# Kernel tuning notes

Measured on AMD Instinct MI355X. Metric: run time of the kernel, lower is better.

The kernel has to match this reference:

```python
import jax, jax.numpy as jnp
import numpy as np

HIDDEN = 16
PROJ = 2
INPUT = 2


def _gates_split(gates):
    # PyTorch LSTM gate order: input, forget, cell(g), output
    i, f, g, o = jnp.split(gates, 4, axis=-1)
    return jax.nn.sigmoid(i), jax.nn.sigmoid(f), jnp.tanh(g), jax.nn.sigmoid(o)


def setup_inputs() -> dict:
    key = jax.random.key(0)
    ks = jax.random.split(key, 7)
    B, T, nstep = 64, 8192, 4096
    bound = 1.0 / np.sqrt(HIDDEN)  # torch default LSTM init: U(-1/sqrt(H), 1/sqrt(H))
    u = lambda k, shp: jax.random.uniform(k, shp, jnp.float32, -bound, bound)
    return {
        "u_train": jax.random.normal(ks[0], (B, T, INPUT), jnp.float32),
        "y_train": jax.random.normal(ks[1], (B, T, INPUT), jnp.float32),
        "W_ih": u(ks[2], (4 * HIDDEN, INPUT)),   # weight_ih_l0
        "W_hh": u(ks[3], (4 * HIDDEN, PROJ)),    # weight_hh_l0 (proj_size -> input to gates)
        "b_ih": u(ks[4], (4 * HIDDEN,)),
        "b_hh": u(ks[5], (4 * HIDDEN,)),
        "W_hr": u(ks[6], (PROJ, HIDDEN)),        # projection weight_hr_l0
        "nstep": nstep,
    }


def reference(u_train, y_train, W_ih, W_hh, b_ih, b_hh, W_hr, nstep):
    b = b_ih + b_hh

    # --- estimate_state: each of the nstep single-step LSTM calls starts from
    # ZERO state (the original never threads state back in), so there is no
    # recurrence: vectorize over all nstep timesteps at once.
    x = y_train[:, :nstep, :]                       # [B, nstep, 2]
    gates = jnp.einsum("bti,gi->btg", x, W_ih) + b  # [B, nstep, 4H]; h-term is 0
    i, f, g, o = _gates_split(gates)
    c1 = i * g                                      # c0 = 0 => f*c0 vanishes
    y1 = jnp.einsum("bth,ph->btp", o * jnp.tanh(c1), W_hr)  # [B, nstep, PROJ]
    hn = y1[:, -1, :]                               # [B, PROJ]
    cn = c1[:, -1, :]                               # [B, HIDDEN]

    # --- predict_state: true recurrent LSTM with projection over the tail.
    def step(carry, x_t):
        h, c = carry                                # h:[B,PROJ] c:[B,HIDDEN]
        gt = x_t @ W_ih.T + h @ W_hh.T + b          # [B, 4H]
        i, f, g, o = _gates_split(gt)
        c = f * c + i * g
        h = (o * jnp.tanh(c)) @ W_hr.T              # [B, PROJ]
        return (h, c), h

    xs = jnp.swapaxes(u_train[:, nstep:, :], 0, 1)  # [T-nstep, B, 2]
    _, ys = jax.lax.scan(step, (hn, cn), xs)
    y2 = jnp.swapaxes(ys, 0, 1)                     # [B, T-nstep, PROJ]

    return jnp.concatenate([y1, y2], axis=1)        # [B, T, PROJ]
```

## Files before the change

### kernel.cpp

```cpp
#include <hip/hip_runtime.h>


#define BB   64
#define TT   8192
#define NST  4096

static __device__ __forceinline__ float fast_exp2(float x) {
#if __has_builtin(__builtin_amdgcn_exp2f)
  return __builtin_amdgcn_exp2f(x);
#else
  return exp2f(x);
#endif
}
static __device__ __forceinline__ float fast_rcp(float x) {
#if __has_builtin(__builtin_amdgcn_rcpf)
  return __builtin_amdgcn_rcpf(x);
#else
  return 1.0f / x;
#endif
}

template <int CTRL>
static __device__ __forceinline__ float rr_add(float x) {
  int r = __builtin_amdgcn_update_dpp(0, __builtin_bit_cast(int, x), CTRL, 0xF, 0xF, true);
  return x + __builtin_bit_cast(float, r);
}

template <int SEL>
static __device__ __forceinline__ float qperm(float x) {
  int r = __builtin_amdgcn_update_dpp(0, __builtin_bit_cast(int, x), SEL, 0xF, 0xF, true);
  return __builtin_bit_cast(float, r);
}

static __device__ __forceinline__ float rdlane63(float x) {
  return __builtin_bit_cast(float,
      __builtin_amdgcn_readlane(__builtin_bit_cast(int, x), 63));
}

struct SW {
  float w0, w1, wh0, wh1, b;
  float m, n;
  float whr0, whr0m2, whr1, whr1m2;
};

static __device__ __forceinline__ void scan_step(const SW& w, float x0, float x1,
                                                 float& h0, float& h1, float& C) {
  const float bse = fmaf(w.w1, x1, fmaf(w.w0, x0, w.b));
  float s = fmaf(w.wh0, h0, bse);
  s = fmaf(w.wh1, h1, s);
  const float d = fast_rcp(1.f + fast_exp2(s));
  const float a = fmaf(d, w.m, w.n);
  const float gi = qperm<0x00>(a);
  const float gf = qperm<0x55>(a);
  const float gg = qperm<0xAA>(a);
  const float go = qperm<0xFF>(a);
  C = fmaf(gf, C, gi * gg);
  const float o0  = go * w.whr0;
  const float o0m = go * w.whr0m2;
  const float o1  = go * w.whr1;
  const float o1m = go * w.whr1m2;
  const float r2 = fast_rcp(1.f + fast_exp2(C));
  float p0 = fmaf(r2, o0m, o0);
  float p1 = fmaf(r2, o1m, o1);
  p0 = rr_add<0x124>(p0); p1 = rr_add<0x124>(p1);
  p0 = rr_add<0x128>(p0); p1 = rr_add<0x128>(p1);
  p0 = rr_add<0x142>(p0); p1 = rr_add<0x142>(p1);
  p0 = rr_add<0x143>(p0); p1 = rr_add<0x143>(p1);
  h0 = rdlane63(p0);
  h1 = rdlane63(p1);
}

__global__ __launch_bounds__(256) void openlstm_kernel(
    const float* __restrict__ u_train, const float* __restrict__ y_train,
    const float* __restrict__ Wih, const float* __restrict__ Whh,
    const float* __restrict__ bih, const float* __restrict__ bhh,
    const float* __restrict__ Whr, float* __restrict__ out) {
  const int tid = threadIdx.x;
  const float S1 = -1.4426950408889634f;
  const float S2 = -2.8853900817779268f;

  if (blockIdx.x < 16) {
    __builtin_amdgcn_s_setprio(1);
    const int lane = tid & 63;
    const int wv   = tid >> 6;
    const int bb   = blockIdx.x * 4 + wv;
    const int hh   = lane >> 2;
    const int r    = lane & 3;
    const int wrow = r * 16 + hh;
    const bool isg = (r == 2);
    const float sc = isg ? S2 : S1;

    SW w;
    w.w0  = Wih[2 * wrow] * sc;  w.w1  = Wih[2 * wrow + 1] * sc;
    w.wh0 = Whh[2 * wrow] * sc;  w.wh1 = Whh[2 * wrow + 1] * sc;
    w.b   = (bih[wrow] + bhh[wrow]) * sc;
    w.m   = isg ? 5.7707801635558536f : 1.f;
    w.n   = isg ? -2.8853900817779268f : 0.f;
    w.whr0   = Whr[hh];
    w.whr0m2 = -2.f * w.whr0;
    w.whr1   = Whr[16 + hh];
    w.whr1m2 = -2.f * w.whr1;

    float h0 = 0.f, h1 = 0.f, C = 0.f;
    {
      const float2 xv = *(const float2*)(y_train + ((size_t)bb * TT + (NST - 1)) * 2);
      scan_step(w, xv.x, xv.y, h0, h1, C);
    }

    const float* up = u_train + ((size_t)bb * TT + NST) * 2;
    float*       op = out     + ((size_t)bb * TT + NST) * 2;

    float4 xq = *(const float4*)(up);
#pragma unroll 4
    for (int p = 0; p < NST / 2 - 1; ++p) {
      const float4 xn = *(const float4*)(up + (size_t)(p + 1) * 4);
      scan_step(w, xq.x, xq.y, h0, h1, C);
      const float ha0 = h0, ha1 = h1;
      scan_step(w, xq.z, xq.w, h0, h1, C);
      *(float4*)(op + (size_t)p * 4) = make_float4(ha0, ha1, h0, h1);
      xq = xn;
    }
    {
      scan_step(w, xq.x, xq.y, h0, h1, C);
      const float ha0 = h0, ha1 = h1;
      scan_step(w, xq.z, xq.w, h0, h1, C);
      *(float4*)(op + (size_t)(NST / 2 - 1) * 4) = make_float4(ha0, ha1, h0, h1);
    }
  } else {
    const int hh  = tid & 15;
    const int grp = tid >> 4;
    const int gid = (blockIdx.x - 16) * 16 + grp;
    const int bb  = gid >> 12;
    const int t   = gid & (NST - 1);
    const int ri = hh, rg = hh + 32, ro = hh + 48;

    const float wii0 = Wih[2 * ri] * S1, wii1 = Wih[2 * ri + 1] * S1;
    const float wig0 = Wih[2 * rg] * S2, wig1 = Wih[2 * rg + 1] * S2;
    const float wio0 = Wih[2 * ro] * S1, wio1 = Wih[2 * ro + 1] * S1;
    const float bi = (bih[ri] + bhh[ri]) * S1;
    const float bg = (bih[rg] + bhh[rg]) * S2;
    const float bo = (bih[ro] + bhh[ro]) * S1;
    const float whr0 = Whr[hh], whr1 = Whr[16 + hh];

    const float2 xv = *(const float2*)(y_train + ((size_t)bb * TT + t) * 2);
    const float si = fmaf(wii1, xv.y, fmaf(wii0, xv.x, bi));
    const float sg = fmaf(wig1, xv.y, fmaf(wig0, xv.x, bg));
    const float so = fmaf(wio1, xv.y, fmaf(wio0, xv.x, bo));
    const float gi = fast_rcp(1.f + fast_exp2(si));
    const float gg = fmaf(2.f, fast_rcp(1.f + fast_exp2(sg)), -1.f);
    const float go = fast_rcp(1.f + fast_exp2(so));
    const float c1 = gi * gg;
    const float tc = fmaf(-2.f, fast_rcp(1.f + fast_exp2(c1 * 2.8853900817779268f)), 1.f);
    const float v  = go * tc;
    float p0 = v * whr0;
    float p1 = v * whr1;
    p0 = rr_add<0x128>(p0); p1 = rr_add<0x128>(p1);
    p0 = rr_add<0x124>(p0); p1 = rr_add<0x124>(p1);
    p0 = rr_add<0x122>(p0); p1 = rr_add<0x122>(p1);
    p0 = rr_add<0x121>(p0); p1 = rr_add<0x121>(p1);
    if (hh == 0) *(float2*)(out + ((size_t)bb * TT + t) * 2) = make_float2(p0, p1);
  }
}

extern "C" void kernel_launch(void* const* d_in, const int* in_sizes, int n_in,
                              void* d_out, int out_size, void* d_ws, size_t ws_size,
                              hipStream_t stream) {
  const float* u_train = (const float*)d_in[0];
  const float* y_train = (const float*)d_in[1];
  const float* Wih     = (const float*)d_in[2];
  const float* Whh     = (const float*)d_in[3];
  const float* bih     = (const float*)d_in[4];
  const float* bhh     = (const float*)d_in[5];
  const float* Whr     = (const float*)d_in[6];
  float* out = (float*)d_out;

  const int grid = 16 + (BB * NST) / 16;
  openlstm_kernel<<<grid, 256, 0, stream>>>(u_train, y_train, Wih, Whh, bih,
                                            bhh, Whr, out);
}
```

Baseline: 499.0 us.

## Prefetch 8-deep input ring and batch 16 outputs into one coalesced store

The sequential scan now keeps an 8-entry register ring of float4 inputs, so each load is issued eight step-pairs before its use. Each lane also captures one h component per step, and lanes 0-31 write 16 timesteps in a single coalesced store instead of one float4 store per two steps. The s_setprio raise for the scan waves is removed. These changes aim to take load latency and per-step store issue off the latency-bound recurrence chain, at the cost of extra selects per step and more register use.

Measured after the change: 448.1 us. 1.11x faster.

```diff
diff --git a/kernel.cpp b/kernel.cpp
--- a/kernel.cpp
+++ b/kernel.cpp
@@ -80,7 +80,6 @@
   const float S2 = -2.8853900817779268f;
 
   if (blockIdx.x < 16) {
-    __builtin_amdgcn_s_setprio(1);
     const int lane = tid & 63;
     const int wv   = tid >> 6;
     const int bb   = blockIdx.x * 4 + wv;
@@ -107,24 +106,45 @@
       scan_step(w, xv.x, xv.y, h0, h1, C);
     }
 
-    const float* up = u_train + ((size_t)bb * TT + NST) * 2;
-    float*       op = out     + ((size_t)bb * TT + NST) * 2;
-
-    float4 xq = *(const float4*)(up);
-#pragma unroll 4
-    for (int p = 0; p < NST / 2 - 1; ++p) {
-      const float4 xn = *(const float4*)(up + (size_t)(p + 1) * 4);
-      scan_step(w, xq.x, xq.y, h0, h1, C);
-      const float ha0 = h0, ha1 = h1;
-      scan_step(w, xq.z, xq.w, h0, h1, C);
-      *(float4*)(op + (size_t)p * 4) = make_float4(ha0, ha1, h0, h1);
-      xq = xn;
+    const float4* up4 = (const float4*)(u_train + ((size_t)bb * TT + NST) * 2);
+    float*        ob  = out + ((size_t)bb * TT + NST) * 2;
+
+    float4 xb[8];
+#pragma unroll
+    for (int k = 0; k < 8; ++k) xb[k] = up4[k];
+
+    const int  cslot = lane >> 1;
+    const bool odd   = lane & 1;
+    float cap = 0.f;
+
+#pragma unroll 1
+    for (int t = 0; t < NST - 16; t += 16) {
+#pragma unroll
+      for (int kp = 0; kp < 8; ++kp) {
+        const float4 xq = xb[kp];
+        xb[kp] = up4[(t >> 1) + kp + 8];
+        scan_step(w, xq.x, xq.y, h0, h1, C);
+        float hsel = odd ? h1 : h0;
+        cap = (cslot == 2 * kp) ? hsel : cap;
+        scan_step(w, xq.z, xq.w, h0, h1, C);
+        hsel = odd ? h1 : h0;
+        cap = (cslot == 2 * kp + 1) ? hsel : cap;
+      }
+      if (lane < 32) ob[(size_t)t * 2 + lane] = cap;
     }
     {
-      scan_step(w, xq.x, xq.y, h0, h1, C);
-      const float ha0 = h0, ha1 = h1;
-      scan_step(w, xq.z, xq.w, h0, h1, C);
-      *(float4*)(op + (size_t)(NST / 2 - 1) * 4) = make_float4(ha0, ha1, h0, h1);
+      const int t = NST - 16;
+#pragma unroll
+      for (int kp = 0; kp < 8; ++kp) {
+        const float4 xq = xb[kp];
+        scan_step(w, xq.x, xq.y, h0, h1, C);
+        float hsel = odd ? h1 : h0;
+        cap = (cslot == 2 * kp) ? hsel : cap;
+        scan_step(w, xq.z, xq.w, h0, h1, C);
+        hsel = odd ? h1 : h0;
+        cap = (cslot == 2 * kp + 1) ? hsel : cap;
+      }
+      if (lane < 32) ob[(size_t)t * 2 + lane] = cap;
     }
   } else {
     const int hh  = tid & 15;
```
